# Optimization experiments

Hardware: AMD Instinct MI355X
Metric: run time of the kernel (lower is better)

## Reference

```python
import jax, jax.numpy as jnp
import numpy as np

B = 64        # number of jagged segments
LMAX = 1024   # max_seq_len
D = 512       # input feature dim
K = 512       # output feature dim
NW = 128      # number of selectable weight matrices
T = 32768     # total jagged tokens (avg len 512)


def setup_inputs() -> dict:
    rng = np.random.default_rng(0)
    # Monotone offsets with avg segment length T//B = 512, jittered +/-200
    # so every length stays in (0, LMAX].
    offsets = np.arange(B + 1, dtype=np.int64) * (T // B)
    offsets[1:-1] += rng.integers(-200, 200, size=B - 1)
    key = jax.random.key(0)
    k1, k2, k3, k4 = jax.random.split(key, 4)
    jagged = jax.random.normal(k1, (T, D), dtype=jnp.float32)
    weight = jax.random.normal(k2, (NW, D, K), dtype=jnp.float32) * 0.02
    bias = jax.random.normal(k3, (NW, K), dtype=jnp.float32)
    index = jax.random.randint(k4, (B,), 0, NW)
    return {
        "max_seq_len": LMAX,
        "offsets": jnp.asarray(offsets),
        "index": index,
        "jagged": jagged,
        "weight": weight,
        "bias": bias,
    }


def reference(max_seq_len, offsets, index, jagged, weight, bias):
    # out[offsets[b]:offsets[b+1]] = jagged[offsets[b]:offsets[b+1]] @ weight[index[b]] + bias[index[b]]
    T_, Dd = jagged.shape
    Kk = weight.shape[-1]
    starts = offsets[:-1]            # [B]
    ends = offsets[1:]               # [B]
    pos = starts[:, None] + jnp.arange(max_seq_len)[None, :]   # [B, L] global row ids
    valid = pos < ends[:, None]                                # [B, L]
    safe = jnp.where(valid, pos, 0)
    padded = jnp.where(valid[..., None], jagged[safe], 0)      # [B, L, D]
    w = weight[index]                                          # [B, D, K] (index-select)
    b = bias[index]                                            # [B, K]
    out_p = jnp.einsum("bld,bdk->blk", padded, w) + b[:, None, :]  # [B, L, K]
    # Scatter padded result back to jagged layout; invalid slots go to row T_ (dropped).
    scatter_idx = jnp.where(valid, pos, T_)
    out = jnp.zeros((T_ + 1, Kk), jagged.dtype).at[scatter_idx].set(out_p)
    return out[:T_]
```

## Files before the change

### kernel.cpp

```cpp
#include <hip/hip_runtime.h>
#include <hip/hip_bf16.h>

#define D_DIM 512
#define K_DIM 512
#define B_C   64
#define LMAX_C 1024

#define BM 128
#define BN 128
#define BK 64
#define KSTEPS 8
#define ROWT 8
#define COLT 4
#define NWG  (B_C * ROWT * COLT)

typedef __attribute__((ext_vector_type(8))) short bf16x8;
typedef __attribute__((ext_vector_type(4))) float f32x4;

__device__ __forceinline__ short f2bf(float f) {
    union { __hip_bfloat16 h; short s; } u;
    u.h = __float2bfloat16(f);
    return u.s;
}

__device__ __forceinline__ short* lds_addr(short* base, int row, int kbyte) {
    return (short*)((char*)base + row * 128 +
                    (kbyte ^ ((((row & 7) ^ ((row >> 2) & 7))) << 4)));
}

__global__ __launch_bounds__(256, 2) void jbmm_kernel(
    const int* __restrict__ offsets,
    const int* __restrict__ index,
    const float* __restrict__ jagged,
    const float* __restrict__ weight,
    const float* __restrict__ bias,
    float* __restrict__ out)
{
    __shared__ short As[2][BM * BK];
    __shared__ short Bs[2][BN * BK];

    const int bidRaw = blockIdx.x;
    const int bid = (bidRaw & 7) * (NWG / 8) + (bidRaw >> 3);

    const int b   = bid / (ROWT * COLT);
    const int rt  = (bid / COLT) % ROWT;
    const int ct  = bid % COLT;

    const int start = offsets[b];
    const int end   = offsets[b + 1];
    const int m0    = start + rt * BM;
    if (m0 >= end) return;
    const int rows = (end - m0) < BM ? (end - m0) : BM;

    const int idxw = index[b];
    const float* W = weight + (size_t)idxw * D_DIM * K_DIM;
    const int n0 = ct * BN;

    const int tid  = threadIdx.x;
    const int lane = tid & 63;
    const int wid  = tid >> 6;
    const int wr   = wid >> 1;
    const int wc   = wid & 1;
    const int lr   = lane & 15;
    const int lg   = lane >> 4;

    const int arow  = tid >> 3;
    const int acol8 = tid & 7;
    const int n4    = tid & 31;
    const int dq8   = tid >> 5;

    float bias_v[4];
#pragma unroll
    for (int ni = 0; ni < 4; ++ni)
        bias_v[ni] = bias[(size_t)idxw * K_DIM + n0 + wc * 64 + ni * 16 + lr];

    f32x4 acc[4][4];
#pragma unroll
    for (int mi = 0; mi < 4; ++mi)
#pragma unroll
        for (int ni = 0; ni < 4; ++ni)
            acc[mi][ni] = (f32x4){0.f, 0.f, 0.f, 0.f};

    f32x4 aR[8];
    f32x4 bR[8];

#define LOADA(k0_)                                                          \
    {                                                                       \
        _Pragma("unroll")                                                   \
        for (int i = 0; i < 4; ++i) {                                       \
            const int r = arow + 32 * i;                                    \
            f32x4 v0 = (f32x4){0.f,0.f,0.f,0.f};                            \
            f32x4 v1 = (f32x4){0.f,0.f,0.f,0.f};                            \
            if (r < rows) {                                                 \
                const float* p = &jagged[(size_t)(m0 + r) * D_DIM + (k0_) + acol8 * 8]; \
                v0 = *reinterpret_cast<const f32x4*>(p);                    \
                v1 = *reinterpret_cast<const f32x4*>(p + 4);                \
            }                                                               \
            aR[2 * i] = v0; aR[2 * i + 1] = v1;                             \
        }                                                                   \
    }

#define LOADB(k0_)                                                          \
    {                                                                       \
        _Pragma("unroll")                                                   \
        for (int j = 0; j < 8; ++j)                                         \
            bR[j] = *reinterpret_cast<const f32x4*>(                        \
                &W[(size_t)((k0_) + dq8 * 8 + j) * K_DIM + n0 + n4 * 4]);   \
    }

#define CVTSTORE(c_)                                                        \
    {                                                                       \
        _Pragma("unroll")                                                   \
        for (int i = 0; i < 4; ++i) {                                       \
            const int r = arow + 32 * i;                                    \
            bf16x8 w;                                                       \
            w[0] = f2bf(aR[2*i][0]); w[1] = f2bf(aR[2*i][1]);               \
            w[2] = f2bf(aR[2*i][2]); w[3] = f2bf(aR[2*i][3]);               \
            w[4] = f2bf(aR[2*i+1][0]); w[5] = f2bf(aR[2*i+1][1]);           \
            w[6] = f2bf(aR[2*i+1][2]); w[7] = f2bf(aR[2*i+1][3]);           \
            *reinterpret_cast<bf16x8*>(lds_addr(&As[c_][0], r, acol8 * 16)) = w; \
        }                                                                   \
        _Pragma("unroll")                                                   \
        for (int np = 0; np < 4; ++np) {                                    \
            bf16x8 w;                                                       \
            w[0] = f2bf(bR[0][np]); w[1] = f2bf(bR[1][np]);                 \
            w[2] = f2bf(bR[2][np]); w[3] = f2bf(bR[3][np]);                 \
            w[4] = f2bf(bR[4][np]); w[5] = f2bf(bR[5][np]);                 \
            w[6] = f2bf(bR[6][np]); w[7] = f2bf(bR[7][np]);                 \
            *reinterpret_cast<bf16x8*>(lds_addr(&Bs[c_][0], n4 * 4 + np, dq8 * 16)) = w; \
        }                                                                   \
    }

#define COMPUTE(c_)                                                         \
    {                                                                       \
        _Pragma("unroll")                                                   \
        for (int kh = 0; kh < 2; ++kh) {                                    \
            bf16x8 af[4], bfr[4];                                           \
            _Pragma("unroll")                                               \
            for (int mi = 0; mi < 4; ++mi)                                  \
                af[mi] = *reinterpret_cast<bf16x8*>(                        \
                    lds_addr(&As[c_][0], wr * 64 + mi * 16 + lr, kh * 64 + lg * 16)); \
            _Pragma("unroll")                                               \
            for (int ni = 0; ni < 4; ++ni)                                  \
                bfr[ni] = *reinterpret_cast<bf16x8*>(                       \
                    lds_addr(&Bs[c_][0], wc * 64 + ni * 16 + lr, kh * 64 + lg * 16)); \
            _Pragma("unroll")                                               \
            for (int mi = 0; mi < 4; ++mi)                                  \
                _Pragma("unroll")                                           \
                for (int ni = 0; ni < 4; ++ni)                              \
                    acc[mi][ni] = __builtin_amdgcn_mfma_f32_16x16x32_bf16(  \
                        af[mi], bfr[ni], acc[mi][ni], 0, 0, 0);             \
        }                                                                   \
    }

    LOADA(0); LOADB(0);
    CVTSTORE(0);
    LOADA(BK); LOADB(BK);
    __syncthreads();

#pragma unroll
    for (int t = 0; t < KSTEPS; ++t) {
        COMPUTE(t & 1);
        if (t + 1 < KSTEPS) {
            CVTSTORE((t + 1) & 1);
            if (t + 2 < KSTEPS) {
                const int kn = (t + 2) * BK;
                LOADA(kn); LOADB(kn);
            }
            __syncthreads();
        }
    }

#pragma unroll
    for (int mi = 0; mi < 4; ++mi) {
        const int rloc = wr * 64 + mi * 16 + lg * 4;
#pragma unroll
        for (int r = 0; r < 4; ++r) {
            const int rr = rloc + r;
            if (rr < rows) {
#pragma unroll
                for (int ni = 0; ni < 4; ++ni) {
                    out[(size_t)(m0 + rr) * K_DIM + n0 + wc * 64 + ni * 16 + lr] =
                        acc[mi][ni][r] + bias_v[ni];
                }
            }
        }
    }
}

extern "C" void kernel_launch(void* const* d_in, const int* in_sizes, int n_in,
                              void* d_out, int out_size, void* d_ws, size_t ws_size,
                              hipStream_t stream) {
    const int*   offsets = (const int*)d_in[1];
    const int*   index   = (const int*)d_in[2];
    const float* jagged  = (const float*)d_in[3];
    const float* weight  = (const float*)d_in[4];
    const float* bias    = (const float*)d_in[5];
    float*       out     = (float*)d_out;

    dim3 grid(NWG);
    dim3 block(256);
    hipLaunchKernelGGL(jbmm_kernel, grid, block, 0, stream,
                       offsets, index, jagged, weight, bias, out);
}
```

Before: 47.66 us.

## Enlarge GEMM tiles to 256x256 with 512-thread blocks and reshape prefetch

Result: slower. 121.8 us (+155.6%).

```diff
diff --git a/kernel.cpp b/kernel.cpp
--- a/kernel.cpp
+++ b/kernel.cpp
@@ -6,12 +6,12 @@
 #define B_C   64
 #define LMAX_C 1024
 
-#define BM 128
-#define BN 128
+#define BM 256
+#define BN 256
 #define BK 64
 #define KSTEPS 8
-#define ROWT 8
-#define COLT 4
+#define ROWT 4
+#define COLT 2
 #define NWG  (B_C * ROWT * COLT)
 
 typedef __attribute__((ext_vector_type(8))) short bf16x8;
@@ -28,7 +28,7 @@
                     (kbyte ^ ((((row & 7) ^ ((row >> 2) & 7))) << 4)));
 }
 
-__global__ __launch_bounds__(256, 2) void jbmm_kernel(
+__global__ __launch_bounds__(512, 2) void jbmm_kernel(
     const int* __restrict__ offsets,
     const int* __restrict__ index,
     const float* __restrict__ jagged,
@@ -59,24 +59,24 @@
     const int tid  = threadIdx.x;
     const int lane = tid & 63;
     const int wid  = tid >> 6;
-    const int wr   = wid >> 1;
-    const int wc   = wid & 1;
+    const int wr   = wid >> 2;
+    const int wc   = wid & 3;
     const int lr   = lane & 15;
     const int lg   = lane >> 4;
 
-    const int arow  = tid >> 3;
-    const int acol8 = tid & 7;
-    const int n4    = tid & 31;
-    const int dq8   = tid >> 5;
+    const int arow  = tid >> 1;
+    const int ahalf = tid & 1;
+    const int nq  = tid & 63;
+    const int ko8 = tid >> 6;
 
     float bias_v[4];
 #pragma unroll
     for (int ni = 0; ni < 4; ++ni)
         bias_v[ni] = bias[(size_t)idxw * K_DIM + n0 + wc * 64 + ni * 16 + lr];
 
-    f32x4 acc[4][4];
-#pragma unroll
-    for (int mi = 0; mi < 4; ++mi)
+    f32x4 acc[8][4];
+#pragma unroll
+    for (int mi = 0; mi < 8; ++mi)
 #pragma unroll
         for (int ni = 0; ni < 4; ++ni)
             acc[mi][ni] = (f32x4){0.f, 0.f, 0.f, 0.f};
@@ -86,17 +86,15 @@
 
 #define LOADA(k0_)                                                          \
     {                                                                       \
-        _Pragma("unroll")                                                   \
-        for (int i = 0; i < 4; ++i) {                                       \
-            const int r = arow + 32 * i;                                    \
-            f32x4 v0 = (f32x4){0.f,0.f,0.f,0.f};                            \
-            f32x4 v1 = (f32x4){0.f,0.f,0.f,0.f};                            \
-            if (r < rows) {                                                 \
-                const float* p = &jagged[(size_t)(m0 + r) * D_DIM + (k0_) + acol8 * 8]; \
-                v0 = *reinterpret_cast<const f32x4*>(p);                    \
-                v1 = *reinterpret_cast<const f32x4*>(p + 4);                \
-            }                                                               \
-            aR[2 * i] = v0; aR[2 * i + 1] = v1;                             \
+        if (arow < rows) {                                                  \
+            const float* p = &jagged[(size_t)(m0 + arow) * D_DIM + (k0_) + ahalf * 32]; \
+            _Pragma("unroll")                                               \
+            for (int j = 0; j < 8; ++j)                                     \
+                aR[j] = *reinterpret_cast<const f32x4*>(p + 4 * j);         \
+        } else {                                                            \
+            _Pragma("unroll")                                               \
+            for (int j = 0; j < 8; ++j)                                     \
+                aR[j] = (f32x4){0.f, 0.f, 0.f, 0.f};                        \
         }                                                                   \
     }
 
@@ -105,20 +103,20 @@
         _Pragma("unroll")                                                   \
         for (int j = 0; j < 8; ++j)                                         \
             bR[j] = *reinterpret_cast<const f32x4*>(                        \
-                &W[(size_t)((k0_) + dq8 * 8 + j) * K_DIM + n0 + n4 * 4]);   \
+                &W[(size_t)((k0_) + ko8 * 8 + j) * K_DIM + n0 + nq * 4]);   \
     }
 
 #define CVTSTORE(c_)                                                        \
     {                                                                       \
         _Pragma("unroll")                                                   \
-        for (int i = 0; i < 4; ++i) {                                       \
-            const int r = arow + 32 * i;                                    \
+        for (int q = 0; q < 4; ++q) {                                       \
             bf16x8 w;                                                       \
-            w[0] = f2bf(aR[2*i][0]); w[1] = f2bf(aR[2*i][1]);               \
-            w[2] = f2bf(aR[2*i][2]); w[3] = f2bf(aR[2*i][3]);               \
-            w[4] = f2bf(aR[2*i+1][0]); w[5] = f2bf(aR[2*i+1][1]);           \
-            w[6] = f2bf(aR[2*i+1][2]); w[7] = f2bf(aR[2*i+1][3]);           \
-            *reinterpret_cast<bf16x8*>(lds_addr(&As[c_][0], r, acol8 * 16)) = w; \
+            w[0] = f2bf(aR[2*q][0]); w[1] = f2bf(aR[2*q][1]);               \
+            w[2] = f2bf(aR[2*q][2]); w[3] = f2bf(aR[2*q][3]);               \
+            w[4] = f2bf(aR[2*q+1][0]); w[5] = f2bf(aR[2*q+1][1]);           \
+            w[6] = f2bf(aR[2*q+1][2]); w[7] = f2bf(aR[2*q+1][3]);           \
+            *reinterpret_cast<bf16x8*>(                                     \
+                lds_addr(&As[c_][0], arow, ahalf * 64 + q * 16)) = w;       \
         }                                                                   \
         _Pragma("unroll")                                                   \
         for (int np = 0; np < 4; ++np) {                                    \
@@ -127,7 +125,8 @@
             w[2] = f2bf(bR[2][np]); w[3] = f2bf(bR[3][np]);                 \
             w[4] = f2bf(bR[4][np]); w[5] = f2bf(bR[5][np]);                 \
             w[6] = f2bf(bR[6][np]); w[7] = f2bf(bR[7][np]);                 \
-            *reinterpret_cast<bf16x8*>(lds_addr(&Bs[c_][0], n4 * 4 + np, dq8 * 16)) = w; \
+            *reinterpret_cast<bf16x8*>(                                     \
+                lds_addr(&Bs[c_][0], nq * 4 + np, ko8 * 16)) = w;           \
         }                                                                   \
     }
 
@@ -135,45 +134,43 @@
     {                                                                       \
         _Pragma("unroll")                                                   \
         for (int kh = 0; kh < 2; ++kh) {                                    \
-            bf16x8 af[4], bfr[4];                                           \
-            _Pragma("unroll")                                               \
-            for (int mi = 0; mi < 4; ++mi)                                  \
-                af[mi] = *reinterpret_cast<bf16x8*>(                        \
-                    lds_addr(&As[c_][0], wr * 64 + mi * 16 + lr, kh * 64 + lg * 16)); \
+            bf16x8 bfr[4];                                                  \
             _Pragma("unroll")                                               \
             for (int ni = 0; ni < 4; ++ni)                                  \
                 bfr[ni] = *reinterpret_cast<bf16x8*>(                       \
                     lds_addr(&Bs[c_][0], wc * 64 + ni * 16 + lr, kh * 64 + lg * 16)); \
             _Pragma("unroll")                                               \
-            for (int mi = 0; mi < 4; ++mi)                                  \
+            for (int mi = 0; mi < 8; ++mi) {                                \
+                bf16x8 af = *reinterpret_cast<bf16x8*>(                     \
+                    lds_addr(&As[c_][0], wr * 128 + mi * 16 + lr, kh * 64 + lg * 16)); \
                 _Pragma("unroll")                                           \
                 for (int ni = 0; ni < 4; ++ni)                              \
                     acc[mi][ni] = __builtin_amdgcn_mfma_f32_16x16x32_bf16(  \
-                        af[mi], bfr[ni], acc[mi][ni], 0, 0, 0);             \
+                        af, bfr[ni], acc[mi][ni], 0, 0, 0);                 \
+            }                                                               \
         }                                                                   \
     }
 
     LOADA(0); LOADB(0);
     CVTSTORE(0);
-    LOADA(BK); LOADB(BK);
     __syncthreads();
 
 #pragma unroll
     for (int t = 0; t < KSTEPS; ++t) {
+        if (t + 1 < KSTEPS) {
+            const int kn = (t + 1) * BK;
+            LOADA(kn); LOADB(kn);
+        }
         COMPUTE(t & 1);
         if (t + 1 < KSTEPS) {
             CVTSTORE((t + 1) & 1);
-            if (t + 2 < KSTEPS) {
-                const int kn = (t + 2) * BK;
-                LOADA(kn); LOADB(kn);
-            }
             __syncthreads();
         }
     }
 
 #pragma unroll
-    for (int mi = 0; mi < 4; ++mi) {
-        const int rloc = wr * 64 + mi * 16 + lg * 4;
+    for (int mi = 0; mi < 8; ++mi) {
+        const int rloc = wr * 128 + mi * 16 + lg * 4;
 #pragma unroll
         for (int r = 0; r < 4; ++r) {
             const int rr = rloc + r;
@@ -199,7 +196,7 @@
     float*       out     = (float*)d_out;
 
     dim3 grid(NWG);
-    dim3 block(256);
+    dim3 block(512);
     hipLaunchKernelGGL(jbmm_kernel, grid, block, 0, stream,
                        offsets, index, jagged, weight, bias, out);
 }
```
